# Performance work log

Measured on AMD Instinct MI355X. Metric: run time of the kernel, lower is better.

Reference implementation:

```python
import jax, jax.numpy as jnp
import numpy as np

K = 2  # top-k experts per token


def setup_inputs() -> dict:
    key = jax.random.key(0)
    kx, kw = jax.random.split(key)
    x = jax.random.normal(kx, (4, 4096, 4096), dtype=jnp.float32)
    W = jax.random.normal(kw, (64, 4096), dtype=jnp.float32) * (4096 ** -0.5)
    return {"x": x, "W": W}


def reference(x, W):
    # gate: logits[b,s,e] = x[b,s,d] @ W[e,d]^T
    logits = jnp.einsum('bsd,ed->bse', x, W)
    scores, idx = jax.lax.top_k(logits, K)           # [B,S,K], [B,S,K]
    probs = jax.nn.softmax(scores, axis=-1)          # softmax over the k selected experts
    return probs, idx
```

## Files before the change

kernel.cpp:

```cpp
#include <hip/hip_runtime.h>
#include <math.h>


typedef float f32x4 __attribute__((ext_vector_type(4)));
typedef short bf16x8 __attribute__((ext_vector_type(8)));
typedef unsigned int u32;

#define NE 64
#define TOK 64
#define CK 128
#define THREADS 512
#define LDE 68

__device__ __forceinline__ u32 cvtpk(float lo, float hi) {
  u32 r;
  asm("v_cvt_pk_bf16_f32 %0, %1, %2" : "=v"(r) : "v"(lo), "v"(hi));
  return r;
}
__device__ __forceinline__ float asf(u32 u) {
  return __builtin_bit_cast(float, u);
}
__device__ __forceinline__ void cvt8(const f32x4 a, const f32x4 b,
                                     uint4& hp, uint4& lp) {
  hp.x = cvtpk(a.x, a.y);
  hp.y = cvtpk(a.z, a.w);
  hp.z = cvtpk(b.x, b.y);
  hp.w = cvtpk(b.z, b.w);
  lp.x = cvtpk(a.x - asf(hp.x << 16), a.y - asf(hp.x & 0xFFFF0000u));
  lp.y = cvtpk(a.z - asf(hp.y << 16), a.w - asf(hp.y & 0xFFFF0000u));
  lp.z = cvtpk(b.x - asf(hp.z << 16), b.y - asf(hp.z & 0xFFFF0000u));
  lp.w = cvtpk(b.z - asf(hp.w << 16), b.w - asf(hp.w & 0xFFFF0000u));
}
__device__ __forceinline__ void gload16(const void* gsrc, void* ldst) {
  __builtin_amdgcn_global_load_lds(
      (const __attribute__((address_space(1))) void*)gsrc,
      (__attribute__((address_space(3))) void*)ldst, 16, 0, 0);
}

__global__ __launch_bounds__(256)
void wprep(const float* __restrict__ Wg, uint2* __restrict__ Who,
           uint2* __restrict__ Wlo) {
  const int i = blockIdx.x * 256 + threadIdx.x;
  const f32x4 v = *((const f32x4*)Wg + i);
  uint2 hp, lp;
  hp.x = cvtpk(v.x, v.y);
  hp.y = cvtpk(v.z, v.w);
  lp.x = cvtpk(v.x - asf(hp.x << 16), v.y - asf(hp.x & 0xFFFF0000u));
  lp.y = cvtpk(v.z - asf(hp.y << 16), v.w - asf(hp.y & 0xFFFF0000u));
  Who[i] = hp;
  Wlo[i] = lp;
}

__global__ __launch_bounds__(THREADS, 2)
void gemm_topk(const float* __restrict__ x, const u32* __restrict__ Whg,
               const u32* __restrict__ Wlg, float* __restrict__ out_probs,
               float* __restrict__ out_idx, int D) {
  __shared__ __align__(16) char smem[98304];

  const int tid = threadIdx.x;
  const int w   = tid >> 6;
  const int l   = tid & 63;
  const int kw  = w & 3;
  const int eh  = w >> 2;
  const int m0  = blockIdx.x * TOK;
  const int nCh = D / CK;
  const int Du  = D / 2;

  const int g   = l >> 4;
  const int r16 = l & 15;

  const int rbase = 2 * w + (l >> 5);
  const int bsw   = (l & 31) ^ (rbase & 7);
  const float* gX = x + (size_t)(m0 + rbase) * D + bsw * 4;
  const size_t jstep = (size_t)16 * D;

  const u32* wh0 = Whg + (size_t)(eh * 32 + 0  + r16) * Du + kw * 16 + g * 4;
  const u32* wh1 = Whg + (size_t)(eh * 32 + 16 + r16) * Du + kw * 16 + g * 4;
  const u32* wl0 = Wlg + (size_t)(eh * 32 + 0  + r16) * Du + kw * 16 + g * 4;
  const u32* wl1 = Wlg + (size_t)(eh * 32 + 16 + r16) * Du + kw * 16 + g * 4;

  const int c0 = kw * 8 + g * 2;
  int aoff[4][2];
#pragma unroll
  for (int m = 0; m < 4; ++m) {
    const int row = m * 16 + r16;
    aoff[m][0] = row * 512 + ((c0       ^ (r16 & 7)) << 4);
    aoff[m][1] = row * 512 + (((c0 + 1) ^ (r16 & 7)) << 4);
  }

  f32x4 acc[4][2];
#pragma unroll
  for (int m = 0; m < 4; ++m)
#pragma unroll
    for (int n = 0; n < 2; ++n) acc[m][n] = (f32x4){0.f, 0.f, 0.f, 0.f};

#pragma unroll
  for (int j = 0; j < 4; ++j)
    gload16(gX + jstep * j, smem + j * 8192 + w * 1024);
#pragma unroll
  for (int j = 0; j < 4; ++j)
    gload16(gX + jstep * j + CK, smem + 32768 + j * 8192 + w * 1024);
  asm volatile("s_waitcnt vmcnt(4)\n\ts_barrier" ::: "memory");

  for (int c = 0; c < nCh; ++c) {
    const int rb = (c % 3) * 32768;

    const size_t ko = (size_t)c * (CK / 2);
    const bf16x8 bh0 = *(const bf16x8*)(wh0 + ko);
    const bf16x8 bh1 = *(const bf16x8*)(wh1 + ko);
    const bf16x8 bl0 = *(const bf16x8*)(wl0 + ko);
    const bf16x8 bl1 = *(const bf16x8*)(wl1 + ko);

    if (c + 2 < nCh) {
      const int wb = ((c + 2) % 3) * 32768;
      const size_t co = (size_t)(c + 2) * CK;
#pragma unroll
      for (int j = 0; j < 4; ++j)
        gload16(gX + co + jstep * j, smem + wb + j * 8192 + w * 1024);
    }

    bf16x8 ah[4], al[4];
#pragma unroll
    for (int m = 0; m < 4; ++m) {
      const f32x4 t0 = *(const f32x4*)(smem + rb + aoff[m][0]);
      const f32x4 t1 = *(const f32x4*)(smem + rb + aoff[m][1]);
      uint4 hp, lp;
      cvt8(t0, t1, hp, lp);
      ah[m] = __builtin_bit_cast(bf16x8, hp);
      al[m] = __builtin_bit_cast(bf16x8, lp);
    }
#pragma unroll
    for (int m = 0; m < 4; ++m) {
      acc[m][0] = __builtin_amdgcn_mfma_f32_16x16x32_bf16(ah[m], bh0, acc[m][0], 0, 0, 0);
      acc[m][0] = __builtin_amdgcn_mfma_f32_16x16x32_bf16(ah[m], bl0, acc[m][0], 0, 0, 0);
      acc[m][0] = __builtin_amdgcn_mfma_f32_16x16x32_bf16(al[m], bh0, acc[m][0], 0, 0, 0);
      acc[m][1] = __builtin_amdgcn_mfma_f32_16x16x32_bf16(ah[m], bh1, acc[m][1], 0, 0, 0);
      acc[m][1] = __builtin_amdgcn_mfma_f32_16x16x32_bf16(ah[m], bl1, acc[m][1], 0, 0, 0);
      acc[m][1] = __builtin_amdgcn_mfma_f32_16x16x32_bf16(al[m], bh1, acc[m][1], 0, 0, 0);
    }

    asm volatile("s_barrier" ::: "memory");
  }

  __syncthreads();

  float* R = (float*)smem;
#pragma unroll
  for (int m = 0; m < 4; ++m)
#pragma unroll
    for (int n = 0; n < 2; ++n)
#pragma unroll
      for (int r = 0; r < 4; ++r)
        R[w * 2048 + ((m * 2 + n) * 4 + r) * 64 + l] = acc[m][n][r];
  __syncthreads();

  float vals[8];
  int dsti[8];
#pragma unroll
  for (int i = 0; i < 8; ++i) {
    const int j = tid + i * THREADS;
    const int t = j >> 6, e = j & 63;
    const int mm = t >> 4, nn = (e >> 4) & 1, ee = e >> 5;
    const int rr = t & 3;
    const int ll = ((t & 15) >> 2) * 16 + (e & 15);
    float v = 0.f;
#pragma unroll
    for (int k = 0; k < 4; ++k)
      v += R[(ee * 4 + k) * 2048 + ((mm * 2 + nn) * 4 + rr) * 64 + ll];
    vals[i] = v;
    dsti[i] = t * LDE + e;
  }
  __syncthreads();
  float* Lf = (float*)smem;
#pragma unroll
  for (int i = 0; i < 8; ++i) Lf[dsti[i]] = vals[i];
  __syncthreads();

  if (tid < TOK) {
    const float* row = &Lf[tid * LDE];
    float b0 = -INFINITY, b1 = -INFINITY;
    int i0 = 0, i1 = 0;
#pragma unroll
    for (int e = 0; e < NE; ++e) {
      const float val = row[e];
      if (val > b0) { b1 = b0; i1 = i0; b0 = val; i0 = e; }
      else if (val > b1) { b1 = val; i1 = e; }
    }
    const float e1  = expf(b1 - b0);
    const float inv = 1.f / (1.f + e1);
    const int tok = m0 + tid;
    out_probs[tok * 2 + 0] = inv;
    out_probs[tok * 2 + 1] = e1 * inv;
    out_idx[tok * 2 + 0] = (float)i0;
    out_idx[tok * 2 + 1] = (float)i1;
  }
}

#define FEW 8
#define FCK 64
#define FLDT 68
#define FTOK 64
__global__ __launch_bounds__(512, 2)
void router_fused(const float* __restrict__ x, const float* __restrict__ W,
                  float* __restrict__ out_probs, float* __restrict__ out_idx,
                  int D) {
  __shared__ float As[2][FTOK][FLDT];
  const int tid = threadIdx.x;
  const int w = __builtin_amdgcn_readfirstlane(tid >> 6);
  const int lane = tid & 63;
  const int m0 = blockIdx.x * FTOK;
  const int nCh = D / FCK;
  const float* xrow = x + (size_t)(m0 + lane) * D;
  const float* __restrict__ wbase = W + (size_t)(w * FEW) * D;
  float acc[FEW];
#pragma unroll
  for (int e = 0; e < FEW; ++e) acc[e] = 0.f;
  {
    const f32x4 a = *reinterpret_cast<const f32x4*>(xrow + 4 * w);
    const f32x4 b = *reinterpret_cast<const f32x4*>(xrow + 4 * (w + 8));
    *reinterpret_cast<f32x4*>(&As[0][lane][4 * w]) = a;
    *reinterpret_cast<f32x4*>(&As[0][lane][4 * (w + 8)]) = b;
  }
  __syncthreads();
  for (int c = 0; c < nCh; ++c) {
    const int buf = c & 1;
    f32x4 na, nb;
    const bool more = (c + 1 < nCh);
    if (more) {
      const float* xn = xrow + (size_t)(c + 1) * FCK;
      na = *reinterpret_cast<const f32x4*>(xn + 4 * w);
      nb = *reinterpret_cast<const f32x4*>(xn + 4 * (w + 8));
    }
    const float* __restrict__ wp = wbase + (size_t)c * FCK;
#pragma unroll 2
    for (int kk = 0; kk < FCK / 4; ++kk) {
      const f32x4 xvv = *reinterpret_cast<const f32x4*>(&As[buf][lane][kk * 4]);
#pragma unroll
      for (int e = 0; e < FEW; ++e) {
        const f32x4 wv = *reinterpret_cast<const f32x4*>(wp + (size_t)e * D + kk * 4);
        acc[e] = fmaf(xvv.x, wv.x, acc[e]);
        acc[e] = fmaf(xvv.y, wv.y, acc[e]);
        acc[e] = fmaf(xvv.z, wv.z, acc[e]);
        acc[e] = fmaf(xvv.w, wv.w, acc[e]);
      }
    }
    __syncthreads();
    if (more) {
      *reinterpret_cast<f32x4*>(&As[buf ^ 1][lane][4 * w]) = na;
      *reinterpret_cast<f32x4*>(&As[buf ^ 1][lane][4 * (w + 8)]) = nb;
    }
    __syncthreads();
  }
  float* L = &As[0][0][0];
  *reinterpret_cast<f32x4*>(&L[lane * FLDT + w * FEW + 0]) =
      (f32x4){acc[0], acc[1], acc[2], acc[3]};
  *reinterpret_cast<f32x4*>(&L[lane * FLDT + w * FEW + 4]) =
      (f32x4){acc[4], acc[5], acc[6], acc[7]};
  __syncthreads();
  if (tid < FTOK) {
    const float* row = &L[tid * FLDT];
    float b0 = -INFINITY, b1 = -INFINITY;
    int i0 = 0, i1 = 0;
#pragma unroll
    for (int e = 0; e < NE; ++e) {
      const float val = row[e];
      if (val > b0) { b1 = b0; i1 = i0; b0 = val; i0 = e; }
      else if (val > b1) { b1 = val; i1 = e; }
    }
    const float e1 = expf(b1 - b0);
    const float inv = 1.f / (1.f + e1);
    const int tok = m0 + tid;
    out_probs[tok * 2 + 0] = inv;
    out_probs[tok * 2 + 1] = e1 * inv;
    out_idx[tok * 2 + 0] = (float)i0;
    out_idx[tok * 2 + 1] = (float)i1;
  }
}

extern "C" void kernel_launch(void* const* d_in, const int* in_sizes, int n_in,
                              void* d_out, int out_size, void* d_ws, size_t ws_size,
                              hipStream_t stream) {
  const float* x = (const float*)d_in[0];
  const float* W = (const float*)d_in[1];

  const int E = 64;
  const int D = in_sizes[1] / E;
  const int nTok = in_sizes[0] / D;

  float* probs = (float*)d_out;
  float* idxo  = (float*)d_out + (size_t)nTok * 2;

  const size_t wBytes = (size_t)E * D * sizeof(short);
  if (ws_size >= 2 * wBytes) {
    u32* Wh = (u32*)d_ws;
    u32* Wl = (u32*)((char*)d_ws + wBytes);
    hipLaunchKernelGGL(wprep, dim3((E * D / 4) / 256), dim3(256), 0, stream,
                       W, (uint2*)Wh, (uint2*)Wl);
    hipLaunchKernelGGL(gemm_topk, dim3(nTok / TOK), dim3(THREADS), 0, stream,
                       x, Wh, Wl, probs, idxo, D);
  } else {
    hipLaunchKernelGGL(router_fused, dim3(nTok / FTOK), dim3(512), 0, stream,
                       x, W, probs, idxo, D);
  }
}
```

Measured before the change: 75.96 us.

## Double block to 1024 threads, one 16-expert tile per wave

Doubles the workgroup to 16 waves, with each wave now computing a single 16-expert slice instead of two. Per-wave accumulators, B-fragment loads and global X loads per chunk are halved, and the reduction and scatter loops are adjusted to match. The goal is more waves in flight to hide the latency of global and LDS loads and the MFMA chain. The cost is that each A fragment converted from LDS is reused across fewer MFMAs, so conversion and LDS traffic grow relative to compute, and barriers now synchronise more waves.

```diff
diff --git a/kernel.cpp b/kernel.cpp
--- a/kernel.cpp
+++ b/kernel.cpp
@@ -9,7 +9,7 @@
 #define NE 64
 #define TOK 64
 #define CK 128
-#define THREADS 512
+#define THREADS 1024
 #define LDE 68
 
 __device__ __forceinline__ u32 cvtpk(float lo, float hi) {
@@ -51,7 +51,7 @@
   Wlo[i] = lp;
 }
 
-__global__ __launch_bounds__(THREADS, 2)
+__global__ __launch_bounds__(THREADS, 4)
 void gemm_topk(const float* __restrict__ x, const u32* __restrict__ Whg,
                const u32* __restrict__ Wlg, float* __restrict__ out_probs,
                float* __restrict__ out_idx, int D) {
@@ -61,7 +61,7 @@
   const int w   = tid >> 6;
   const int l   = tid & 63;
   const int kw  = w & 3;
-  const int eh  = w >> 2;
+  const int es  = w >> 2;
   const int m0  = blockIdx.x * TOK;
   const int nCh = D / CK;
   const int Du  = D / 2;
@@ -72,12 +72,10 @@
   const int rbase = 2 * w + (l >> 5);
   const int bsw   = (l & 31) ^ (rbase & 7);
   const float* gX = x + (size_t)(m0 + rbase) * D + bsw * 4;
-  const size_t jstep = (size_t)16 * D;
-
-  const u32* wh0 = Whg + (size_t)(eh * 32 + 0  + r16) * Du + kw * 16 + g * 4;
-  const u32* wh1 = Whg + (size_t)(eh * 32 + 16 + r16) * Du + kw * 16 + g * 4;
-  const u32* wl0 = Wlg + (size_t)(eh * 32 + 0  + r16) * Du + kw * 16 + g * 4;
-  const u32* wl1 = Wlg + (size_t)(eh * 32 + 16 + r16) * Du + kw * 16 + g * 4;
+  const size_t jstep = (size_t)32 * D;
+
+  const u32* whb = Whg + (size_t)(es * 16 + r16) * Du + kw * 16 + g * 4;
+  const u32* wlb = Wlg + (size_t)(es * 16 + r16) * Du + kw * 16 + g * 4;
 
   const int c0 = kw * 8 + g * 2;
   int aoff[4][2];
@@ -88,55 +86,44 @@
     aoff[m][1] = row * 512 + (((c0 + 1) ^ (r16 & 7)) << 4);
   }
 
-  f32x4 acc[4][2];
-#pragma unroll
-  for (int m = 0; m < 4; ++m)
-#pragma unroll
-    for (int n = 0; n < 2; ++n) acc[m][n] = (f32x4){0.f, 0.f, 0.f, 0.f};
-
-#pragma unroll
-  for (int j = 0; j < 4; ++j)
-    gload16(gX + jstep * j, smem + j * 8192 + w * 1024);
-#pragma unroll
-  for (int j = 0; j < 4; ++j)
-    gload16(gX + jstep * j + CK, smem + 32768 + j * 8192 + w * 1024);
-  asm volatile("s_waitcnt vmcnt(4)\n\ts_barrier" ::: "memory");
+  f32x4 acc[4];
+#pragma unroll
+  for (int m = 0; m < 4; ++m) acc[m] = (f32x4){0.f, 0.f, 0.f, 0.f};
+
+#pragma unroll
+  for (int j = 0; j < 2; ++j)
+    gload16(gX + jstep * j, smem + j * 16384 + w * 1024);
+#pragma unroll
+  for (int j = 0; j < 2; ++j)
+    gload16(gX + jstep * j + CK, smem + 32768 + j * 16384 + w * 1024);
+  asm volatile("s_waitcnt vmcnt(2)\n\ts_barrier" ::: "memory");
 
   for (int c = 0; c < nCh; ++c) {
     const int rb = (c % 3) * 32768;
 
     const size_t ko = (size_t)c * (CK / 2);
-    const bf16x8 bh0 = *(const bf16x8*)(wh0 + ko);
-    const bf16x8 bh1 = *(const bf16x8*)(wh1 + ko);
-    const bf16x8 bl0 = *(const bf16x8*)(wl0 + ko);
-    const bf16x8 bl1 = *(const bf16x8*)(wl1 + ko);
+    const bf16x8 bh = *(const bf16x8*)(whb + ko);
+    const bf16x8 bl = *(const bf16x8*)(wlb + ko);
 
     if (c + 2 < nCh) {
       const int wb = ((c + 2) % 3) * 32768;
       const size_t co = (size_t)(c + 2) * CK;
 #pragma unroll
-      for (int j = 0; j < 4; ++j)
-        gload16(gX + co + jstep * j, smem + wb + j * 8192 + w * 1024);
-    }
-
-    bf16x8 ah[4], al[4];
+      for (int j = 0; j < 2; ++j)
+        gload16(gX + co + jstep * j, smem + wb + j * 16384 + w * 1024);
+    }
+
 #pragma unroll
     for (int m = 0; m < 4; ++m) {
       const f32x4 t0 = *(const f32x4*)(smem + rb + aoff[m][0]);
       const f32x4 t1 = *(const f32x4*)(smem + rb + aoff[m][1]);
       uint4 hp, lp;
       cvt8(t0, t1, hp, lp);
-      ah[m] = __builtin_bit_cast(bf16x8, hp);
-      al[m] = __builtin_bit_cast(bf16x8, lp);
-    }
-#pragma unroll
-    for (int m = 0; m < 4; ++m) {
-      acc[m][0] = __builtin_amdgcn_mfma_f32_16x16x32_bf16(ah[m], bh0, acc[m][0], 0, 0, 0);
-      acc[m][0] = __builtin_amdgcn_mfma_f32_16x16x32_bf16(ah[m], bl0, acc[m][0], 0, 0, 0);
-      acc[m][0] = __builtin_amdgcn_mfma_f32_16x16x32_bf16(al[m], bh0, acc[m][0], 0, 0, 0);
-      acc[m][1] = __builtin_amdgcn_mfma_f32_16x16x32_bf16(ah[m], bh1, acc[m][1], 0, 0, 0);
-      acc[m][1] = __builtin_amdgcn_mfma_f32_16x16x32_bf16(ah[m], bl1, acc[m][1], 0, 0, 0);
-      acc[m][1] = __builtin_amdgcn_mfma_f32_16x16x32_bf16(al[m], bh1, acc[m][1], 0, 0, 0);
+      const bf16x8 ah = __builtin_bit_cast(bf16x8, hp);
+      const bf16x8 al = __builtin_bit_cast(bf16x8, lp);
+      acc[m] = __builtin_amdgcn_mfma_f32_16x16x32_bf16(ah, bh, acc[m], 0, 0, 0);
+      acc[m] = __builtin_amdgcn_mfma_f32_16x16x32_bf16(ah, bl, acc[m], 0, 0, 0);
+      acc[m] = __builtin_amdgcn_mfma_f32_16x16x32_bf16(al, bh, acc[m], 0, 0, 0);
     }
 
     asm volatile("s_barrier" ::: "memory");
@@ -148,32 +135,31 @@
 #pragma unroll
   for (int m = 0; m < 4; ++m)
 #pragma unroll
-    for (int n = 0; n < 2; ++n)
-#pragma unroll
-      for (int r = 0; r < 4; ++r)
-        R[w * 2048 + ((m * 2 + n) * 4 + r) * 64 + l] = acc[m][n][r];
-  __syncthreads();
-
-  float vals[8];
-  int dsti[8];
-#pragma unroll
-  for (int i = 0; i < 8; ++i) {
+    for (int r = 0; r < 4; ++r)
+      R[w * 1024 + (m * 4 + r) * 64 + l] = acc[m][r];
+  __syncthreads();
+
+  float vals[4];
+  int dsti[4];
+#pragma unroll
+  for (int i = 0; i < 4; ++i) {
     const int j = tid + i * THREADS;
     const int t = j >> 6, e = j & 63;
-    const int mm = t >> 4, nn = (e >> 4) & 1, ee = e >> 5;
-    const int rr = t & 3;
-    const int ll = ((t & 15) >> 2) * 16 + (e & 15);
+    const int ee = e >> 4;
+    const int mm = t >> 4, tr = t & 15;
+    const int ll = (tr >> 2) * 16 + (e & 15);
+    const int ri = (mm * 4 + (tr & 3)) * 64 + ll;
     float v = 0.f;
 #pragma unroll
     for (int k = 0; k < 4; ++k)
-      v += R[(ee * 4 + k) * 2048 + ((mm * 2 + nn) * 4 + rr) * 64 + ll];
+      v += R[(ee * 4 + k) * 1024 + ri];
     vals[i] = v;
     dsti[i] = t * LDE + e;
   }
   __syncthreads();
   float* Lf = (float*)smem;
 #pragma unroll
-  for (int i = 0; i < 8; ++i) Lf[dsti[i]] = vals[i];
+  for (int i = 0; i < 4; ++i) Lf[dsti[i]] = vals[i];
   __syncthreads();
 
   if (tid < TOK) {
```

After: 79.16 us. 4.2% more time.
